# Kernel tuning notes

Hardware: AMD Instinct MI355X
Metric: run time of the kernel (lower is better)

The kernel has to match this reference:

```python
import jax, jax.numpy as jnp
import numpy as np

B, T, D = 8, 4096, 128
NUM_CB, K = 8, 1024


def setup_inputs() -> dict:
    key = jax.random.key(0)
    k1, k2 = jax.random.split(key)
    embeddings = jax.random.normal(k1, (B, T, D), dtype=jnp.float32)
    # nn.init.uniform_(w, -1/codebook_size, 1/codebook_size)
    codebooks = jax.random.uniform(k2, (NUM_CB, K, D), dtype=jnp.float32,
                                   minval=-1.0 / K, maxval=1.0 / K)
    return {"embeddings": embeddings, "codebooks": codebooks}


def reference(embeddings, codebooks):
    """Residual VQ: returns (codes [B,T,C] int32, quantized [B,T,D], commitment_loss scalar)."""
    Bv, Tv, Dv = embeddings.shape
    flat = embeddings.reshape(-1, Dv)  # [N, D]

    def step(carry, cb_w):  # cb_w: [K, D]
        residual, quant, loss = carry
        # squared euclidean distance; argmin identical to torch.cdist argmin
        d2 = (jnp.sum(residual * residual, axis=-1, keepdims=True)
              - 2.0 * (residual @ cb_w.T)
              + jnp.sum(cb_w * cb_w, axis=-1))  # [N, K]
        idx = jnp.argmin(d2, axis=-1)  # [N]
        ql = cb_w[idx]  # [N, D] gather
        loss = loss + jnp.mean((jax.lax.stop_gradient(residual) - ql) ** 2)
        quant = quant + ql
        residual = residual - jax.lax.stop_gradient(ql)
        return (residual, quant, loss), idx

    init = (flat, jnp.zeros_like(flat), jnp.float32(0.0))
    (_, quant, loss), codes = jax.lax.scan(step, init, codebooks)
    codes = codes.T.reshape(Bv, Tv, codebooks.shape[0])  # [C,N] -> [B,T,C]
    quant = quant.reshape(Bv, Tv, Dv)
    # straight-through estimator
    quantized = embeddings + jax.lax.stop_gradient(quant - embeddings)
    return codes, quantized, loss / codebooks.shape[0]
```

## Files before the change

### kernel.cpp

```cpp
#include <hip/hip_runtime.h>


#define N_ROWS 32768
#define DIM    128
#define KCB    1024
#define NCB    8
#define MB     64
#define PC     64
#define NPASS  (KCB / PC)
#define LDA    132

__global__ __launch_bounds__(256) void zero_ws_kernel(double* lws) {
    if (threadIdx.x < NCB) lws[threadIdx.x] = 0.0;
}

__global__ __launch_bounds__(256) void c2_kernel(const float* __restrict__ cbw,
                                                 float* __restrict__ c2g) {
#pragma clang fp contract(off)
    int code = blockIdx.x * 256 + threadIdx.x;
    const float* row = cbw + (size_t)code * DIM;
    float s[8];
    for (int j = 0; j < 8; ++j) { float x = row[j]; s[j] = x * x; }
    for (int m = 1; m < 16; ++m)
        for (int j = 0; j < 8; ++j) { float x = row[m * 8 + j]; float p = x * x; s[j] += p; }
    c2g[code] = ((s[0] + s[1]) + (s[2] + s[3])) + ((s[4] + s[5]) + (s[6] + s[7]));
}

__global__ __launch_bounds__(256, 2) void rvq_kernel(
    const float* __restrict__ emb, const float* __restrict__ cbw,
    const float* __restrict__ c2g, float* __restrict__ out,
    double* __restrict__ lws)
{
    __shared__ float a_lds[MB * LDA];
    __shared__ float b_lds[PC * LDA];
    __shared__ float r2_lds[MB];
    __shared__ float c2_lds[PC];
    __shared__ float scr[4 * MB];
    __shared__ int   codes_lds[NCB * MB];

    const int tid  = threadIdx.x;
    const int tcol = tid & 15;
    const int trow = tid >> 4;
    const size_t base = (size_t)blockIdx.x * MB;

    for (int s = 0; s < 8; ++s) {
        int f4 = s * 256 + tid;
        int r = f4 >> 5, k4 = f4 & 31;
        float4 v = *(const float4*)(emb + (base + r) * DIM + (size_t)k4 * 4);
        *(float4*)(a_lds + r * LDA + k4 * 4) = v;
    }
    __syncthreads();

    {
#pragma clang fp contract(off)
        int r = tid & 63, q = tid >> 6;
        float x0 = a_lds[r * LDA + 2 * q];     float s0 = x0 * x0;
        float x1 = a_lds[r * LDA + 2 * q + 1]; float s1 = x1 * x1;
        for (int m = 1; m < 16; ++m) {
            float y0 = a_lds[r * LDA + m * 8 + 2 * q];     float p0 = y0 * y0; s0 += p0;
            float y1 = a_lds[r * LDA + m * 8 + 2 * q + 1]; float p1 = y1 * y1; s1 += p1;
        }
        scr[q * MB + r] = s0 + s1;
    }
    __syncthreads();
    if (tid < MB) {
#pragma clang fp contract(off)
        float t0 = scr[tid], t1 = scr[MB + tid], t2 = scr[2 * MB + tid], t3 = scr[3 * MB + tid];
        r2_lds[tid] = (t0 + t1) + (t2 + t3);
    }

    float minv[4]; int mini[4];

    for (int cb = 0; cb < NCB; ++cb) {
        const float* cbbase = cbw + (size_t)cb * KCB * DIM;
        for (int i = 0; i < 4; ++i) { minv[i] = 3.4e38f; mini[i] = 0; }

        for (int pass = 0; pass < NPASS; ++pass) {
            __syncthreads();
            const float* bsrc = cbbase + (size_t)pass * PC * DIM;
            for (int s = 0; s < 8; ++s) {
                int f4 = s * 256 + tid;
                int c = f4 >> 5, k4 = f4 & 31;
                float4 v = *(const float4*)(bsrc + (size_t)c * DIM + k4 * 4);
                *(float4*)(b_lds + c * LDA + k4 * 4) = v;
            }
            if (tid < PC) c2_lds[tid] = c2g[cb * KCB + pass * PC + tid];
            __syncthreads();

            float acc[4][4];
            for (int i = 0; i < 4; ++i)
                for (int j = 0; j < 4; ++j) acc[i][j] = 0.f;
#pragma unroll 4
            for (int k4 = 0; k4 < 32; ++k4) {
                float4 av[4], bv[4];
                for (int i = 0; i < 4; ++i)
                    av[i] = *(const float4*)(a_lds + (trow + 16 * i) * LDA + k4 * 4);
                for (int j = 0; j < 4; ++j)
                    bv[j] = *(const float4*)(b_lds + (tcol + 16 * j) * LDA + k4 * 4);
                for (int i = 0; i < 4; ++i)
                    for (int j = 0; j < 4; ++j) {
                        acc[i][j] = fmaf(av[i].x, bv[j].x, acc[i][j]);
                        acc[i][j] = fmaf(av[i].y, bv[j].y, acc[i][j]);
                        acc[i][j] = fmaf(av[i].z, bv[j].z, acc[i][j]);
                        acc[i][j] = fmaf(av[i].w, bv[j].w, acc[i][j]);
                    }
            }
            {
#pragma clang fp contract(off)
                float r2v[4], c2v[4];
                for (int i = 0; i < 4; ++i) r2v[i] = r2_lds[trow + 16 * i];
                for (int j = 0; j < 4; ++j) c2v[j] = c2_lds[tcol + 16 * j];
                for (int i = 0; i < 4; ++i)
                    for (int j = 0; j < 4; ++j) {
                        float t  = r2v[i] - 2.0f * acc[i][j];
                        float d2 = t + c2v[j];
                        int   cg = pass * PC + tcol + 16 * j;
                        if (d2 < minv[i]) { minv[i] = d2; mini[i] = cg; }
                    }
            }
        }

        for (int i = 0; i < 4; ++i) {
            float v = minv[i]; int ix = mini[i];
            for (int m = 1; m <= 8; m <<= 1) {
                float v2 = __shfl_xor(v, m, 64);
                int  ix2 = __shfl_xor(ix, m, 64);
                if (v2 < v || (v2 == v && ix2 < ix)) { v = v2; ix = ix2; }
            }
            if (tcol == 0) codes_lds[cb * MB + (trow + 16 * i)] = ix;
        }
        __syncthreads();

        {
#pragma clang fp contract(off)
            int r = tid & 63, q = tid >> 6;
            int widx = codes_lds[cb * MB + r];
            const float* ql = cbbase + (size_t)widx * DIM;
            float s0 = 0.f, s1 = 0.f;
            double lacc = 0.0;
            for (int m = 0; m < 16; ++m) {
                int k0 = m * 8 + 2 * q;
                float a0 = a_lds[r * LDA + k0];
                float q0 = ql[k0];
                float n0 = a0 - q0;
                a_lds[r * LDA + k0] = n0;
                float p0 = n0 * n0;
                if (m == 0) s0 = p0; else s0 += p0;
                lacc += (double)p0;
                int k1 = k0 + 1;
                float a1 = a_lds[r * LDA + k1];
                float q1 = ql[k1];
                float n1 = a1 - q1;
                a_lds[r * LDA + k1] = n1;
                float p1 = n1 * n1;
                if (m == 0) s1 = p1; else s1 += p1;
                lacc += (double)p1;
            }
            scr[q * MB + r] = s0 + s1;
            for (int off = 32; off > 0; off >>= 1) lacc += __shfl_down(lacc, off, 64);
            if ((tid & 63) == 0) atomicAdd(&lws[cb], lacc);
        }
        __syncthreads();
        if (tid < MB) {
#pragma clang fp contract(off)
            float t0 = scr[tid], t1 = scr[MB + tid], t2 = scr[2 * MB + tid], t3 = scr[3 * MB + tid];
            r2_lds[tid] = (t0 + t1) + (t2 + t3);
        }
    }
    __syncthreads();

    if (tid < MB) {
        int r = tid;
        float4 u, v;
        u.x = (float)codes_lds[0 * MB + r]; u.y = (float)codes_lds[1 * MB + r];
        u.z = (float)codes_lds[2 * MB + r]; u.w = (float)codes_lds[3 * MB + r];
        v.x = (float)codes_lds[4 * MB + r]; v.y = (float)codes_lds[5 * MB + r];
        v.z = (float)codes_lds[6 * MB + r]; v.w = (float)codes_lds[7 * MB + r];
        *(float4*)(out + (base + r) * NCB)     = u;
        *(float4*)(out + (base + r) * NCB + 4) = v;
    }

    {
#pragma clang fp contract(off)
        int r = tid >> 2, q4 = tid & 3;
        size_t rg = base + r;
        int cds[NCB];
        for (int cb = 0; cb < NCB; ++cb) cds[cb] = codes_lds[cb * MB + r];
        float* qout = out + (size_t)N_ROWS * NCB;
        for (int ii = 0; ii < 8; ++ii) {
            int k = q4 * 32 + ii * 4;
            float4 qv = make_float4(0.f, 0.f, 0.f, 0.f);
            for (int cb = 0; cb < NCB; ++cb) {
                float4 cv = *(const float4*)(cbw + ((size_t)cb * KCB + cds[cb]) * DIM + k);
                qv.x += cv.x; qv.y += cv.y; qv.z += cv.z; qv.w += cv.w;
            }
            float4 ev = *(const float4*)(emb + rg * DIM + k);
            float4 ov;
            ov.x = ev.x + (qv.x - ev.x);
            ov.y = ev.y + (qv.y - ev.y);
            ov.z = ev.z + (qv.z - ev.z);
            ov.w = ev.w + (qv.w - ev.w);
            *(float4*)(qout + rg * DIM + k) = ov;
        }
    }
}

__global__ __launch_bounds__(64) void finish_loss_kernel(const double* __restrict__ lws,
                                                         float* __restrict__ out_loss) {
    if (threadIdx.x == 0 && blockIdx.x == 0) {
        float l = 0.f;
        for (int cb = 0; cb < NCB; ++cb) {
            float m = (float)(lws[cb] / 4194304.0);
            l = l + m;
        }
        out_loss[0] = l / 8.0f;
    }
}

extern "C" void kernel_launch(void* const* d_in, const int* in_sizes, int n_in,
                              void* d_out, int out_size, void* d_ws, size_t ws_size,
                              hipStream_t stream) {
    const float* emb = (const float*)d_in[0];
    const float* cbw = (const float*)d_in[1];
    float* out = (float*)d_out;
    double* lws = (double*)d_ws;
    float* c2g = (float*)((char*)d_ws + 256);

    hipLaunchKernelGGL(zero_ws_kernel, dim3(1), dim3(64), 0, stream, lws);
    hipLaunchKernelGGL(c2_kernel, dim3(32), dim3(256), 0, stream, cbw, c2g);
    hipLaunchKernelGGL(rvq_kernel, dim3(512), dim3(256), 0, stream, emb, cbw, c2g, out, lws);
    hipLaunchKernelGGL(finish_loss_kernel, dim3(1), dim3(64), 0, stream, lws,
                       out + (size_t)N_ROWS * NCB + (size_t)N_ROWS * DIM);
}
```

Before: 1.197 ms.

## Restructure RVQ distance GEMM to per-wave code slices read from global

Each block now runs 512 threads in 8 waves. Each wave owns a 16-code slice per pass, and each lane computes one row against those codes, reading codebook values directly from global memory instead of staging them in LDS. This removes the per-pass LDS staging and its two barriers per pass, and replaces the shuffle-based argmin with a cross-wave LDS reduction. The loss is now written to per-block slots and summed in the finish kernel instead of using atomics, which also removes the zeroing kernel. In exchange, the inner loop does many scalar global loads that are uniform across the wave, and arithmetic intensity per thread drops from a 4x4 register tile to 1x16.

```diff
diff --git a/kernel.cpp b/kernel.cpp
--- a/kernel.cpp
+++ b/kernel.cpp
@@ -5,14 +5,13 @@
 #define DIM    128
 #define KCB    1024
 #define NCB    8
+#define LDA    132
+
 #define MB     64
-#define PC     64
-#define NPASS  (KCB / PC)
-#define LDA    132
-
-__global__ __launch_bounds__(256) void zero_ws_kernel(double* lws) {
-    if (threadIdx.x < NCB) lws[threadIdx.x] = 0.0;
-}
+#define CW     16
+#define PCODES 128
+#define NPASS  (KCB / PCODES)
+#define NBLK   (N_ROWS / MB)
 
 __global__ __launch_bounds__(256) void c2_kernel(const float* __restrict__ cbw,
                                                  float* __restrict__ c2g) {
@@ -26,25 +25,27 @@
     c2g[code] = ((s[0] + s[1]) + (s[2] + s[3])) + ((s[4] + s[5]) + (s[6] + s[7]));
 }
 
-__global__ __launch_bounds__(256, 2) void rvq_kernel(
+__global__ __launch_bounds__(512) void rvq_kernel(
     const float* __restrict__ emb, const float* __restrict__ cbw,
     const float* __restrict__ c2g, float* __restrict__ out,
-    double* __restrict__ lws)
+    double* __restrict__ slots)
 {
-    __shared__ float a_lds[MB * LDA];
-    __shared__ float b_lds[PC * LDA];
-    __shared__ float r2_lds[MB];
-    __shared__ float c2_lds[PC];
-    __shared__ float scr[4 * MB];
-    __shared__ int   codes_lds[NCB * MB];
+    __shared__ float  a_lds[MB * LDA];
+    __shared__ float  c2_lds[KCB];
+    __shared__ float  r2_lds[MB];
+    __shared__ float  scrP[8 * MB];
+    __shared__ float  scrF[8 * MB];
+    __shared__ int    scrI[8 * MB];
+    __shared__ double scrL[8];
+    __shared__ int    codes_lds[NCB * MB];
 
     const int tid  = threadIdx.x;
-    const int tcol = tid & 15;
-    const int trow = tid >> 4;
+    const int lane = tid & 63;
+    const int wv   = __builtin_amdgcn_readfirstlane(tid >> 6);
     const size_t base = (size_t)blockIdx.x * MB;
 
-    for (int s = 0; s < 8; ++s) {
-        int f4 = s * 256 + tid;
+    for (int s = 0; s < 4; ++s) {
+        int f4 = s * 512 + tid;
         int r = f4 >> 5, k4 = f4 & 31;
         float4 v = *(const float4*)(emb + (base + r) * DIM + (size_t)k4 * 4);
         *(float4*)(a_lds + r * LDA + k4 * 4) = v;
@@ -54,80 +55,83 @@
     {
 #pragma clang fp contract(off)
         int r = tid & 63, q = tid >> 6;
-        float x0 = a_lds[r * LDA + 2 * q];     float s0 = x0 * x0;
-        float x1 = a_lds[r * LDA + 2 * q + 1]; float s1 = x1 * x1;
+        float x = a_lds[r * LDA + q]; float sq = x * x;
         for (int m = 1; m < 16; ++m) {
-            float y0 = a_lds[r * LDA + m * 8 + 2 * q];     float p0 = y0 * y0; s0 += p0;
-            float y1 = a_lds[r * LDA + m * 8 + 2 * q + 1]; float p1 = y1 * y1; s1 += p1;
-        }
-        scr[q * MB + r] = s0 + s1;
+            float y = a_lds[r * LDA + m * 8 + q]; float p = y * y; sq += p;
+        }
+        scrP[q * MB + r] = sq;
     }
     __syncthreads();
     if (tid < MB) {
 #pragma clang fp contract(off)
-        float t0 = scr[tid], t1 = scr[MB + tid], t2 = scr[2 * MB + tid], t3 = scr[3 * MB + tid];
-        r2_lds[tid] = (t0 + t1) + (t2 + t3);
-    }
-
-    float minv[4]; int mini[4];
+        float s0 = scrP[tid],          s1 = scrP[MB + tid];
+        float s2 = scrP[2 * MB + tid], s3 = scrP[3 * MB + tid];
+        float s4 = scrP[4 * MB + tid], s5 = scrP[5 * MB + tid];
+        float s6 = scrP[6 * MB + tid], s7 = scrP[7 * MB + tid];
+        r2_lds[tid] = ((s0 + s1) + (s2 + s3)) + ((s4 + s5) + (s6 + s7));
+    }
+
+    const float* ar = a_lds + lane * LDA;
 
     for (int cb = 0; cb < NCB; ++cb) {
         const float* cbbase = cbw + (size_t)cb * KCB * DIM;
-        for (int i = 0; i < 4; ++i) { minv[i] = 3.4e38f; mini[i] = 0; }
+
+        if (tid < 256) {
+            float4 cv = *(const float4*)(c2g + cb * KCB + tid * 4);
+            *(float4*)(c2_lds + tid * 4) = cv;
+        }
+        __syncthreads();
+
+        float minv = 3.4e38f; int mini = 0;
+        const float r2v = r2_lds[lane];
 
         for (int pass = 0; pass < NPASS; ++pass) {
-            __syncthreads();
-            const float* bsrc = cbbase + (size_t)pass * PC * DIM;
-            for (int s = 0; s < 8; ++s) {
-                int f4 = s * 256 + tid;
-                int c = f4 >> 5, k4 = f4 & 31;
-                float4 v = *(const float4*)(bsrc + (size_t)c * DIM + k4 * 4);
-                *(float4*)(b_lds + c * LDA + k4 * 4) = v;
-            }
-            if (tid < PC) c2_lds[tid] = c2g[cb * KCB + pass * PC + tid];
-            __syncthreads();
-
-            float acc[4][4];
-            for (int i = 0; i < 4; ++i)
-                for (int j = 0; j < 4; ++j) acc[i][j] = 0.f;
-#pragma unroll 4
+            const int c0 = pass * PCODES + wv * CW;
+            const float* __restrict__ bw = cbbase + (size_t)c0 * DIM;
+
+            float acc[CW];
+#pragma unroll
+            for (int c = 0; c < CW; ++c) acc[c] = 0.f;
+
+#pragma unroll 2
             for (int k4 = 0; k4 < 32; ++k4) {
-                float4 av[4], bv[4];
-                for (int i = 0; i < 4; ++i)
-                    av[i] = *(const float4*)(a_lds + (trow + 16 * i) * LDA + k4 * 4);
-                for (int j = 0; j < 4; ++j)
-                    bv[j] = *(const float4*)(b_lds + (tcol + 16 * j) * LDA + k4 * 4);
-                for (int i = 0; i < 4; ++i)
-                    for (int j = 0; j < 4; ++j) {
-                        acc[i][j] = fmaf(av[i].x, bv[j].x, acc[i][j]);
-                        acc[i][j] = fmaf(av[i].y, bv[j].y, acc[i][j]);
-                        acc[i][j] = fmaf(av[i].z, bv[j].z, acc[i][j]);
-                        acc[i][j] = fmaf(av[i].w, bv[j].w, acc[i][j]);
-                    }
+                float4 av = *(const float4*)(ar + k4 * 4);
+                const float* __restrict__ bk = bw + k4 * 4;
+#pragma unroll
+                for (int c = 0; c < CW; ++c) {
+                    float b0 = bk[c * DIM + 0];
+                    float b1 = bk[c * DIM + 1];
+                    float b2 = bk[c * DIM + 2];
+                    float b3 = bk[c * DIM + 3];
+                    acc[c] = fmaf(av.x, b0, acc[c]);
+                    acc[c] = fmaf(av.y, b1, acc[c]);
+                    acc[c] = fmaf(av.z, b2, acc[c]);
+                    acc[c] = fmaf(av.w, b3, acc[c]);
+                }
             }
             {
 #pragma clang fp contract(off)
-                float r2v[4], c2v[4];
-                for (int i = 0; i < 4; ++i) r2v[i] = r2_lds[trow + 16 * i];
-                for (int j = 0; j < 4; ++j) c2v[j] = c2_lds[tcol + 16 * j];
-                for (int i = 0; i < 4; ++i)
-                    for (int j = 0; j < 4; ++j) {
-                        float t  = r2v[i] - 2.0f * acc[i][j];
-                        float d2 = t + c2v[j];
-                        int   cg = pass * PC + tcol + 16 * j;
-                        if (d2 < minv[i]) { minv[i] = d2; mini[i] = cg; }
-                    }
-            }
-        }
-
-        for (int i = 0; i < 4; ++i) {
-            float v = minv[i]; int ix = mini[i];
-            for (int m = 1; m <= 8; m <<= 1) {
-                float v2 = __shfl_xor(v, m, 64);
-                int  ix2 = __shfl_xor(ix, m, 64);
+#pragma unroll
+                for (int c = 0; c < CW; ++c) {
+                    float t  = r2v - 2.0f * acc[c];
+                    float d2 = t + c2_lds[c0 + c];
+                    int   cg = c0 + c;
+                    if (d2 < minv) { minv = d2; mini = cg; }
+                }
+            }
+        }
+
+        scrF[wv * MB + lane] = minv;
+        scrI[wv * MB + lane] = mini;
+        __syncthreads();
+        if (tid < MB) {
+            float v = scrF[tid]; int ix = scrI[tid];
+            for (int w = 1; w < 8; ++w) {
+                float v2 = scrF[w * MB + tid];
+                int  ix2 = scrI[w * MB + tid];
                 if (v2 < v || (v2 == v && ix2 < ix)) { v = v2; ix = ix2; }
             }
-            if (tcol == 0) codes_lds[cb * MB + (trow + 16 * i)] = ix;
+            codes_lds[cb * MB + tid] = ix;
         }
         __syncthreads();
 
@@ -136,35 +140,35 @@
             int r = tid & 63, q = tid >> 6;
             int widx = codes_lds[cb * MB + r];
             const float* ql = cbbase + (size_t)widx * DIM;
-            float s0 = 0.f, s1 = 0.f;
+            float sq = 0.f;
             double lacc = 0.0;
             for (int m = 0; m < 16; ++m) {
-                int k0 = m * 8 + 2 * q;
-                float a0 = a_lds[r * LDA + k0];
-                float q0 = ql[k0];
-                float n0 = a0 - q0;
-                a_lds[r * LDA + k0] = n0;
-                float p0 = n0 * n0;
-                if (m == 0) s0 = p0; else s0 += p0;
-                lacc += (double)p0;
-                int k1 = k0 + 1;
-                float a1 = a_lds[r * LDA + k1];
-                float q1 = ql[k1];
-                float n1 = a1 - q1;
-                a_lds[r * LDA + k1] = n1;
-                float p1 = n1 * n1;
-                if (m == 0) s1 = p1; else s1 += p1;
-                lacc += (double)p1;
-            }
-            scr[q * MB + r] = s0 + s1;
+                int k = m * 8 + q;
+                float a = a_lds[r * LDA + k];
+                float qv = ql[k];
+                float n = a - qv;
+                a_lds[r * LDA + k] = n;
+                float p = n * n;
+                if (m == 0) sq = p; else sq += p;
+                lacc += (double)p;
+            }
+            scrP[q * MB + r] = sq;
             for (int off = 32; off > 0; off >>= 1) lacc += __shfl_down(lacc, off, 64);
-            if ((tid & 63) == 0) atomicAdd(&lws[cb], lacc);
-        }
-        __syncthreads();
+            if (lane == 0) scrL[wv] = lacc;
+        }
+        __syncthreads();
+        if (tid == 0) {
+            double s = 0.0;
+            for (int w = 0; w < 8; ++w) s += scrL[w];
+            slots[(size_t)blockIdx.x * NCB + cb] = s;
+        }
         if (tid < MB) {
 #pragma clang fp contract(off)
-            float t0 = scr[tid], t1 = scr[MB + tid], t2 = scr[2 * MB + tid], t3 = scr[3 * MB + tid];
-            r2_lds[tid] = (t0 + t1) + (t2 + t3);
+            float s0 = scrP[tid],          s1 = scrP[MB + tid];
+            float s2 = scrP[2 * MB + tid], s3 = scrP[3 * MB + tid];
+            float s4 = scrP[4 * MB + tid], s5 = scrP[5 * MB + tid];
+            float s6 = scrP[6 * MB + tid], s7 = scrP[7 * MB + tid];
+            r2_lds[tid] = ((s0 + s1) + (s2 + s3)) + ((s4 + s5) + (s6 + s7));
         }
     }
     __syncthreads();
@@ -182,13 +186,13 @@
 
     {
 #pragma clang fp contract(off)
-        int r = tid >> 2, q4 = tid & 3;
+        int r = tid >> 3, q8 = tid & 7;
         size_t rg = base + r;
         int cds[NCB];
         for (int cb = 0; cb < NCB; ++cb) cds[cb] = codes_lds[cb * MB + r];
         float* qout = out + (size_t)N_ROWS * NCB;
-        for (int ii = 0; ii < 8; ++ii) {
-            int k = q4 * 32 + ii * 4;
+        for (int ii = 0; ii < 4; ++ii) {
+            int k = q8 * 16 + ii * 4;
             float4 qv = make_float4(0.f, 0.f, 0.f, 0.f);
             for (int cb = 0; cb < NCB; ++cb) {
                 float4 cv = *(const float4*)(cbw + ((size_t)cb * KCB + cds[cb]) * DIM + k);
@@ -205,12 +209,14 @@
     }
 }
 
-__global__ __launch_bounds__(64) void finish_loss_kernel(const double* __restrict__ lws,
+__global__ __launch_bounds__(64) void finish_loss_kernel(const double* __restrict__ slots,
                                                          float* __restrict__ out_loss) {
     if (threadIdx.x == 0 && blockIdx.x == 0) {
         float l = 0.f;
         for (int cb = 0; cb < NCB; ++cb) {
-            float m = (float)(lws[cb] / 4194304.0);
+            double s = 0.0;
+            for (int b = 0; b < NBLK; ++b) s += slots[(size_t)b * NCB + cb];
+            float m = (float)(s / 4194304.0);
             l = l + m;
         }
         out_loss[0] = l / 8.0f;
@@ -223,12 +229,12 @@
     const float* emb = (const float*)d_in[0];
     const float* cbw = (const float*)d_in[1];
     float* out = (float*)d_out;
-    double* lws = (double*)d_ws;
-    float* c2g = (float*)((char*)d_ws + 256);
-
-    hipLaunchKernelGGL(zero_ws_kernel, dim3(1), dim3(64), 0, stream, lws);
+    double* slots = (double*)d_ws;
+    float* c2g = (float*)((char*)d_ws + 32768);
+
     hipLaunchKernelGGL(c2_kernel, dim3(32), dim3(256), 0, stream, cbw, c2g);
-    hipLaunchKernelGGL(rvq_kernel, dim3(512), dim3(256), 0, stream, emb, cbw, c2g, out, lws);
-    hipLaunchKernelGGL(finish_loss_kernel, dim3(1), dim3(64), 0, stream, lws,
+    hipLaunchKernelGGL(rvq_kernel, dim3(NBLK), dim3(512), 0, stream,
+                       emb, cbw, c2g, out, slots);
+    hipLaunchKernelGGL(finish_loss_kernel, dim3(1), dim3(64), 0, stream, slots,
                        out + (size_t)N_ROWS * NCB + (size_t)N_ROWS * DIM);
 }
```

After: 1.835 ms. +53.2%, slower.
